# Optimization experiments

Hardware: AMD Instinct MI355X
Metric: run time of the kernel (lower is better)

Reference implementation:

```python
import jax, jax.numpy as jnp
import numpy as np
from jax import lax

D_MODEL = 256
VOCAB = 512
D_INNER = 512          # expand=2
D_STATE = 64
D_CONV = 4
HEADDIM = 32
NHEADS = D_INNER // HEADDIM  # 16
NGROUPS = 1
CHUNK = 64
D_IN_PROJ = 2 * D_INNER + 2 * NGROUPS * D_STATE + NHEADS  # 1168
CONV_DIM = D_INNER + 2 * NGROUPS * D_STATE               # 640


def setup_inputs() -> dict:
    key = jax.random.key(0)
    ks = jax.random.split(key, 8)
    B, L = 8, 4096
    input_ids = jax.random.randint(ks[0], (B, L), 0, VOCAB)
    rn = lambda k, shp, sc: (jax.random.normal(k, shp) * sc).astype(jnp.float32)
    embed_w = rn(ks[1], (VOCAB, D_MODEL), 0.02).at[0].set(0.0)  # padding_idx=0
    in_proj_w = rn(ks[2], (D_IN_PROJ, D_MODEL), D_MODEL ** -0.5)
    conv_w = rn(ks[3], (CONV_DIM, D_CONV), 0.2)
    conv_b = jnp.zeros((CONV_DIM,), jnp.float32)
    A_log = jnp.log(jax.random.uniform(ks[4], (NHEADS,), minval=1.0, maxval=16.0)).astype(jnp.float32)
    D_skip = jnp.ones((NHEADS,), jnp.float32)
    dt0 = jax.random.uniform(ks[5], (NHEADS,), minval=1e-3, maxval=0.1)
    dt_bias = jnp.log(jnp.expm1(dt0)).astype(jnp.float32)  # inverse softplus
    gate_norm_w = jnp.ones((D_INNER,), jnp.float32)
    out_proj_w = rn(ks[6], (D_MODEL, D_INNER), D_INNER ** -0.5)
    norm_w = jnp.ones((D_MODEL,), jnp.float32)
    return dict(input_ids=input_ids, embed_w=embed_w, in_proj_w=in_proj_w,
                conv_w=conv_w, conv_b=conv_b, A_log=A_log, D_skip=D_skip,
                dt_bias=dt_bias, gate_norm_w=gate_norm_w, out_proj_w=out_proj_w,
                norm_w=norm_w)


def _rmsnorm(x, w, eps):
    return x * lax.rsqrt(jnp.mean(x * x, axis=-1, keepdims=True) + eps) * w


def _segsum(a):
    # a: (..., T) -> (..., T, T); out[q,s] = sum_{s+1..q} a, -inf above diag
    T = a.shape[-1]
    c = jnp.cumsum(a, axis=-1)
    seg = c[..., :, None] - c[..., None, :]
    mask = jnp.tril(jnp.ones((T, T), bool))
    return jnp.where(mask, seg, -jnp.inf)


def _ssd(X, A, Bm, Cm):
    # X:(b,l,h,p) already *dt ; A:(b,l,h)=dt*A_head ; Bm,Cm:(b,l,n)
    b, l, h, p = X.shape
    n = Bm.shape[-1]
    c, q = l // CHUNK, CHUNK
    X = X.reshape(b, c, q, h, p)
    A = A.reshape(b, c, q, h).transpose(0, 3, 1, 2)        # (b,h,c,q)
    Bm = Bm.reshape(b, c, q, n)
    Cm = Cm.reshape(b, c, q, n)
    A_cs = jnp.cumsum(A, axis=-1)                           # (b,h,c,q)
    Lmat = jnp.exp(_segsum(A))                              # (b,h,c,q,q)
    # intra-chunk (diagonal block) output
    Y_diag = jnp.einsum('bcqn,bckn,bhcqk,bckhp->bcqhp', Cm, Bm, Lmat, X)
    # states carried to end of each chunk
    decay_states = jnp.exp(A_cs[..., -1:] - A_cs)           # (b,h,c,q)
    states = jnp.einsum('bckn,bhck,bckhp->bchpn', Bm, decay_states, X)
    chunk_decay = jnp.exp(A_cs[..., -1])                    # (b,h,c)
    def step(hprev, inp):
        dec, st = inp
        return dec[..., None, None] * hprev + st, hprev
    _, prev = lax.scan(step, jnp.zeros((b, h, p, n), X.dtype),
                       (chunk_decay.transpose(2, 0, 1), states.transpose(1, 0, 2, 3, 4)))
    prev = prev.transpose(1, 0, 2, 3, 4)                    # (b,c,h,p,n)
    Y_off = jnp.einsum('bcqn,bchpn,bhcq->bcqhp', Cm, prev, jnp.exp(A_cs))
    return (Y_diag + Y_off).reshape(b, l, h, p)


def _mamba2(u, in_proj_w, conv_w, conv_b, A_log, D_skip, dt_bias, gate_norm_w, out_proj_w):
    B, L, _ = u.shape
    zxbcdt = u @ in_proj_w.T                                # (B,L,1168)
    z = zxbcdt[..., :D_INNER]
    xBC = zxbcdt[..., D_INNER:D_INNER + CONV_DIM]
    dt = zxbcdt[..., D_INNER + CONV_DIM:]                   # (B,L,H)
    # causal depthwise conv + silu
    xBC = lax.conv_general_dilated(xBC.transpose(0, 2, 1), conv_w[:, None, :],
                                   (1,), [(D_CONV - 1, 0)],
                                   dimension_numbers=('NCH', 'OIH', 'NCH'),
                                   feature_group_count=CONV_DIM)
    xBC = jax.nn.silu(xBC + conv_b[None, :, None]).transpose(0, 2, 1)
    x = xBC[..., :D_INNER].reshape(B, L, NHEADS, HEADDIM)
    Bm = xBC[..., D_INNER:D_INNER + D_STATE]
    Cm = xBC[..., D_INNER + D_STATE:]
    dt = jax.nn.softplus(dt + dt_bias)                      # (B,L,H)
    A = -jnp.exp(A_log)                                     # (H,)
    y = _ssd(x * dt[..., None], dt * A, Bm, Cm)
    y = y + D_skip[None, None, :, None] * x
    y = y.reshape(B, L, D_INNER)
    y = _rmsnorm(y * jax.nn.silu(z), gate_norm_w, 1e-5)     # RMSNormGated
    return y @ out_proj_w.T


def reference(input_ids, embed_w, in_proj_w, conv_w, conv_b, A_log, D_skip,
              dt_bias, gate_norm_w, out_proj_w, norm_w):
    x = embed_w[input_ids]                                  # (B,L,D)
    u = _rmsnorm(x, norm_w, 1e-6)
    x = x + _mamba2(u, in_proj_w, conv_w, conv_b, A_log, D_skip,
                    dt_bias, gate_norm_w, out_proj_w)
    logits = x @ embed_w.T                                  # tied lm_head
    return logits
```

## Files before the change

### kernel.cpp

```cpp
#include <hip/hip_runtime.h>
#include <cstdint>
#include <cstddef>

#define TOK    32768
#define BATCH  8
#define SEQ    4096
#define DMODEL 256
#define DINNER 512
#define DSTATE 64
#define NH     16
#define HD     32
#define DPROJ  1168
#define NPAD   1280
#define CONVD  640
#define VOCAB  512
#define HGRP   4
#define TS     132

typedef __attribute__((ext_vector_type(8))) short bf16x8;
typedef __attribute__((ext_vector_type(4))) float f32x4;

__device__ __forceinline__ unsigned short f2bf(float f) {
    unsigned u = __float_as_uint(f);
    u += 0x7fffu + ((u >> 16) & 1u);
    return (unsigned short)(u >> 16);
}
__device__ __forceinline__ float bf2f(short s) {
    return __uint_as_float(((unsigned)(unsigned short)s) << 16);
}
__device__ __forceinline__ unsigned cvtpk(float lo, float hi) {
    unsigned r;
    asm("v_cvt_pk_bf16_f32 %0, %1, %2" : "=v"(r) : "v"(lo), "v"(hi));
    return r;
}
__device__ __forceinline__ float fsilu(float s) {
    return s * __builtin_amdgcn_rcpf(1.f + __expf(-s));
}
__device__ __forceinline__ float sp(float v) {
    return v > 20.f ? v : __logf(1.f + __expf(v));
}

__device__ __forceinline__ void gload16(const short* src, short* dst) {
    __builtin_amdgcn_global_load_lds((const __attribute__((address_space(1))) void*)src,
                                     (__attribute__((address_space(3))) void*)dst, 16, 0, 0);
}

#define U16_OFF   0
#define Z16_OFF   (U16_OFF  + (size_t)TOK*128)
#define XBC_OFF   (Z16_OFF  + (size_t)TOK*256)
#define DTS_OFF   (XBC_OFF  + (size_t)TOK*320)
#define ACS_OFF   (DTS_OFF  + (size_t)TOK*16)
#define CDEC_OFF  (ACS_OFF  + (size_t)BATCH*NH*64*64)
#define WP_OFF    (CDEC_OFF + (size_t)BATCH*NH*64)
#define WO_OFF    (WP_OFF   + 163840)
#define WE_OFF    (WO_OFF   + 65536)
#define UNION_OFF (WE_OFF   + 65536)
#define UNION_FL  ((size_t)BATCH*64*NH*2048)
#define Y16_SUB   ((size_t)TOK*256)
#define XF_SUB    ((size_t)TOK*256)
#define WS_FLOATS (UNION_OFF + UNION_FL)

__global__ void k_diag(float* out, float wsmb) {
    if (blockIdx.x == 0 && threadIdx.x == 0) out[0] = wsmb;
}

__global__ void k_cvt(const float* __restrict__ s, short* __restrict__ d, int nsrc, int ntot) {
    int i = blockIdx.x * 256 + threadIdx.x;
    if (i < ntot) d[i] = (i < nsrc) ? (short)f2bf(s[i]) : (short)0;
}

__global__ void k_embed(const int* __restrict__ ids, const float* __restrict__ embed,
                        const float* __restrict__ norm_w, short* __restrict__ u16) {
    int t = blockIdx.x;
    int lane = threadIdx.x;
    int id = ids[t];
    float4 v = ((const float4*)(embed + (size_t)id * DMODEL))[lane];
    float ss = v.x*v.x + v.y*v.y + v.z*v.z + v.w*v.w;
    #pragma unroll
    for (int o = 32; o > 0; o >>= 1) ss += __shfl_down(ss, o);
    ss = __shfl(ss, 0);
    float r = rsqrtf(ss * (1.0f / DMODEL) + 1e-6f);
    float4 w = ((const float4*)norm_w)[lane];
    unsigned p0 = cvtpk(v.x * r * w.x, v.y * r * w.y);
    unsigned p1 = cvtpk(v.z * r * w.z, v.w * r * w.w);
    ((uint2*)(u16 + (size_t)t * DMODEL))[lane] = make_uint2(p0, p1);
}

template<int MODE>
__global__ __launch_bounds__(512) void k_gemm_mfma(
    const short* __restrict__ A, const short* __restrict__ B, int K,
    float* __restrict__ outF, short* __restrict__ z16, short* __restrict__ xbc,
    float* __restrict__ dts, const float* __restrict__ dt_bias,
    const int* __restrict__ ids, const float* __restrict__ embed,
    const float* __restrict__ cw, const float* __restrict__ cb) {
    __shared__ __align__(16) short SM[32768];
    int tid = threadIdx.x;
    int m0 = blockIdx.y << 7;
    int n0 = blockIdx.x << 7;
    int wave = tid >> 6, lane = tid & 63;
    int wm = wave >> 1, wn = wave & 1;
    int lr = lane & 15, lg = lane >> 4;
    const f32x4 zer = {0.f, 0.f, 0.f, 0.f};
    f32x4 acc[2][4];
    #pragma unroll
    for (int i = 0; i < 2; i++)
        #pragma unroll
        for (int j = 0; j < 4; j++) acc[i][j] = zer;

    const bool isXBC = (MODE == 0) && (n0 >= 512) && (n0 < 1152);
    const bool atStart = (m0 & (SEQ - 1)) == 0;
    const bool haloLane = isXBC && (wm == 0) && !atStart && (lr < 3);
    f32x4 hacc[4];
    #pragma unroll
    for (int j = 0; j < 4; j++) hacc[j] = zer;
    const bf16x8 hz = {0, 0, 0, 0, 0, 0, 0, 0};
    bf16x8 hc0 = hz, hc1 = hz, hn0 = hz, hn1 = hz;

    const int nK = K >> 6;
    const int slo = lane >> 3;
    const int skb = ((lane & 7) ^ slo) << 3;

    {
        #pragma unroll
        for (int j = 0; j < 2; j++) {
            int row = wave * 16 + j * 8 + slo;
            gload16(A + (size_t)(m0 + row) * K + skb, SM + (wave * 2 + j) * 512);
            gload16(B + (size_t)(n0 + row) * K + skb, SM + 16384 + (wave * 2 + j) * 512);
        }
        if (haloLane) {
            hc0 = *(const bf16x8*)(A + (size_t)(m0 - 3 + lr) * K + lg * 8);
            hc1 = *(const bf16x8*)(A + (size_t)(m0 - 3 + lr) * K + 32 + lg * 8);
        }
    }
    __syncthreads();

    for (int kt = 0; kt < nK; ++kt) {
        if (kt + 1 < nK) {
            int k0 = (kt + 1) << 6;
            int nb = ((kt + 1) & 1) * 8192;
            #pragma unroll
            for (int j = 0; j < 2; j++) {
                int row = wave * 16 + j * 8 + slo;
                gload16(A + (size_t)(m0 + row) * K + k0 + skb, SM + nb + (wave * 2 + j) * 512);
                gload16(B + (size_t)(n0 + row) * K + k0 + skb, SM + 16384 + nb + (wave * 2 + j) * 512);
            }
            if (haloLane) {
                hn0 = *(const bf16x8*)(A + (size_t)(m0 - 3 + lr) * K + k0 + lg * 8);
                hn1 = *(const bf16x8*)(A + (size_t)(m0 - 3 + lr) * K + k0 + 32 + lg * 8);
            }
        }
        const short* CA = SM + (kt & 1) * 8192;
        const short* CB = SM + 16384 + (kt & 1) * 8192;
        #pragma unroll
        for (int kk = 0; kk < 2; kk++) {
            int sw = (((kk << 2) + lg) ^ (lr & 7)) << 3;
            bf16x8 af[2], bfr[4];
            #pragma unroll
            for (int mi = 0; mi < 2; mi++)
                af[mi] = *(const bf16x8*)&CA[(wm * 32 + mi * 16 + lr) * 64 + sw];
            #pragma unroll
            for (int ni = 0; ni < 4; ni++)
                bfr[ni] = *(const bf16x8*)&CB[(wn * 64 + ni * 16 + lr) * 64 + sw];
            #pragma unroll
            for (int mi = 0; mi < 2; mi++)
                #pragma unroll
                for (int ni = 0; ni < 4; ni++)
                    acc[mi][ni] = __builtin_amdgcn_mfma_f32_16x16x32_bf16(af[mi], bfr[ni], acc[mi][ni], 0, 0, 0);
            if (isXBC && wm == 0) {
                bf16x8 h = (kk == 0) ? hc0 : hc1;
                #pragma unroll
                for (int ni = 0; ni < 4; ni++)
                    hacc[ni] = __builtin_amdgcn_mfma_f32_16x16x32_bf16(h, bfr[ni], hacc[ni], 0, 0, 0);
            }
        }
        __syncthreads();
        hc0 = hn0; hc1 = hn1;
    }

    if (isXBC) {
        short* Tile = SM;
        #pragma unroll
        for (int mi = 0; mi < 2; mi++)
            #pragma unroll
            for (int ni = 0; ni < 4; ni++)
                #pragma unroll
                for (int r = 0; r < 4; r++) {
                    int row = wm * 32 + mi * 16 + lg * 4 + r;
                    int col = wn * 64 + ni * 16 + lr;
                    float v = acc[mi][ni][r];
                    float vo = __shfl_xor(v, 1);
                    if (!(lr & 1))
                        *(unsigned*)&Tile[(3 + row) * TS + col] = cvtpk(v, vo);
                }
        if (wm == 0 && lg == 0) {
            #pragma unroll
            for (int ni = 0; ni < 4; ni++)
                #pragma unroll
                for (int r = 0; r < 3; r++)
                    Tile[r * TS + wn * 64 + ni * 16 + lr] = (short)f2bf(hacc[ni][r]);
        }
        __syncthreads();
        int cp = tid & 63, rg = tid >> 6;
        int colb = cp * 2;
        int ch = (n0 - 512) + colb;
        float c0w0 = cw[ch * 4], c0w1 = cw[ch * 4 + 1], c0w2 = cw[ch * 4 + 2], c0w3 = cw[ch * 4 + 3];
        float c1w0 = cw[ch * 4 + 4], c1w1 = cw[ch * 4 + 5], c1w2 = cw[ch * 4 + 6], c1w3 = cw[ch * 4 + 7];
        float b0v = cb[ch], b1v = cb[ch + 1];
        int rbase = rg * 16;
        unsigned w0 = *(const unsigned*)&Tile[(rbase + 0) * TS + colb];
        unsigned w1 = *(const unsigned*)&Tile[(rbase + 1) * TS + colb];
        unsigned w2 = *(const unsigned*)&Tile[(rbase + 2) * TS + colb];
        for (int i = 0; i < 16; i++) {
            unsigned w3 = *(const unsigned*)&Tile[(rbase + i + 3) * TS + colb];
            float s0 = b0v, s1 = b1v;
            s0 = fmaf(bf2f((short)(w0 & 0xffffu)), c0w0, s0); s1 = fmaf(bf2f((short)(w0 >> 16)), c1w0, s1);
            s0 = fmaf(bf2f((short)(w1 & 0xffffu)), c0w1, s0); s1 = fmaf(bf2f((short)(w1 >> 16)), c1w1, s1);
            s0 = fmaf(bf2f((short)(w2 & 0xffffu)), c0w2, s0); s1 = fmaf(bf2f((short)(w2 >> 16)), c1w2, s1);
            s0 = fmaf(bf2f((short)(w3 & 0xffffu)), c0w3, s0); s1 = fmaf(bf2f((short)(w3 >> 16)), c1w3, s1);
            s0 = fsilu(s0);
            s1 = fsilu(s1);
            *(unsigned*)&xbc[(size_t)(m0 + rbase + i) * CONVD + ch] = cvtpk(s0, s1);
            w0 = w1; w1 = w2; w2 = w3;
        }
        return;
    }

    #pragma unroll
    for (int mi = 0; mi < 2; mi++) {
        #pragma unroll
        for (int r = 0; r < 4; r++) {
            int row = m0 + wm * 32 + mi * 16 + lg * 4 + r;
            int id = 0;
            if (MODE == 1) id = ids[row];
            #pragma unroll
            for (int ni = 0; ni < 4; ni++) {
                int col = n0 + wn * 64 + ni * 16 + lr;
                float v = acc[mi][ni][r];
                if (MODE == 0) {
                    if (n0 < 512) {
                        float vo = __shfl_xor(v, 1);
                        if (!(lr & 1))
                            *(unsigned*)&z16[(size_t)row * DINNER + col] = cvtpk(v, vo);
                    } else if (wn == 0 && ni == 0) {
                        dts[(size_t)row * NH + lr] = sp(v + dt_bias[lr]);
                    }
                } else if (MODE == 1) {
                    float vo = __shfl_xor(v, 1);
                    if (!(lr & 1)) {
                        float2 res = *(const float2*)&embed[(size_t)id * DMODEL + col];
                        *(unsigned*)&z16[(size_t)row * DMODEL + col] = cvtpk(v + res.x, vo + res.y);
                    }
                } else {
                    outF[(size_t)row * VOCAB + col] = v;
                }
            }
        }
    }
}

__global__ __launch_bounds__(256) void k_states(const short* __restrict__ xbc, const float* __restrict__ dts,
                                                const float* __restrict__ A_log,
                                                short* __restrict__ st16,
                                                float* __restrict__ acs_g, float* __restrict__ cdec) {
    __shared__ short BsB[64 * 72];
    __shared__ short BT[64 * 72];
    __shared__ short Xd0[32 * 72];
    __shared__ short Xd1[32 * 72];
    __shared__ float dkS[HGRP][64];
    int tid = threadIdx.x;
    int bid = blockIdx.x;
    int hg = bid & 3;
    int bc = bid >> 2;
    int b = bc >> 6, c = bc & 63;
    int h0 = hg * HGRP;
    size_t tbase = (size_t)b * SEQ + (size_t)c * 64;
    int wave = tid >> 6, lane = tid & 63;
    int lr = lane & 15, lg = lane >> 4;

    for (int i = tid; i < 64 * 64; i += 256) {
        int q = i >> 6, n = i & 63;
        BsB[q * 72 + n] = xbc[(tbase + q) * CONVD + DINNER + n];
    }
    {
        int h = h0 + wave;
        float Ah = -__expf(A_log[h]);
        float v = dts[(tbase + lane) * NH + h] * Ah;
        #pragma unroll
        for (int off = 1; off < 64; off <<= 1) {
            float o = __shfl_up(v, off);
            if (lane >= off) v += o;
        }
        acs_g[(((size_t)(b * NH + h)) * 64 + c) * 64 + lane] = v;
        float alast = __shfl(v, 63);
        dkS[wave][lane] = __expf(alast - v);
        if (lane == 0) cdec[(b * NH + h) * 64 + c] = __expf(alast);
    }
    __syncthreads();
    for (int i = tid; i < 64 * 64; i += 256) {
        int k = i >> 6, n = i & 63;
        BT[n * 72 + k] = BsB[k * 72 + n];
    }
    __syncthreads();

    auto do_head = [&](int h, const short* Xd) {
        int ptile = wave & 1;
        bf16x8 a0 = *(const bf16x8*)&Xd[(ptile * 16 + lr) * 72 + lg * 8];
        bf16x8 a1 = *(const bf16x8*)&Xd[(ptile * 16 + lr) * 72 + 32 + lg * 8];
        size_t base = ((size_t)bc * NH + h) * 2048;
        #pragma unroll
        for (int j = 0; j < 2; j++) {
            int nt = (wave >> 1) * 2 + j;
            bf16x8 b0 = *(const bf16x8*)&BT[(nt * 16 + lr) * 72 + lg * 8];
            bf16x8 b1 = *(const bf16x8*)&BT[(nt * 16 + lr) * 72 + 32 + lg * 8];
            f32x4 z = {0.f, 0.f, 0.f, 0.f};
            z = __builtin_amdgcn_mfma_f32_16x16x32_bf16(a0, b0, z, 0, 0, 0);
            z = __builtin_amdgcn_mfma_f32_16x16x32_bf16(a1, b1, z, 0, 0, 0);
            #pragma unroll
            for (int r = 0; r < 4; r++) {
                int p = ptile * 16 + lg * 4 + r;
                float v = z[r];
                float vo = __shfl_xor(v, 1);
                if (!(lr & 1))
                    *(unsigned*)&st16[base + p * 64 + nt * 16 + lr] = cvtpk(v, vo);
            }
        }
    };

    #pragma unroll
    for (int pr = 0; pr < HGRP / 2; pr++) {
        int hhA = pr * 2, hhB = hhA + 1;
        int hA = h0 + hhA, hB = h0 + hhB;
        for (int i = tid; i < 2048; i += 256) {
            int p = i & 31, k = i >> 5;
            float dtA = dts[(tbase + k) * NH + hA];
            float dtB = dts[(tbase + k) * NH + hB];
            Xd0[p * 72 + k] = (short)f2bf(bf2f(xbc[(tbase + k) * CONVD + hA * HD + p]) * dtA * dkS[hhA][k]);
            Xd1[p * 72 + k] = (short)f2bf(bf2f(xbc[(tbase + k) * CONVD + hB * HD + p]) * dtB * dkS[hhB][k]);
        }
        __syncthreads();
        do_head(hA, Xd0);
        do_head(hB, Xd1);
        __syncthreads();
    }
}

__global__ __launch_bounds__(256) void k_scan(unsigned* __restrict__ st32, const float* __restrict__ cdec) {
    int bid = blockIdx.x;
    int bh = bid >> 2, seg = bid & 3;
    int b = bh >> 4, h = bh & 15;
    int off = seg * 256 + threadIdx.x;
    float p0 = 0.f, p1 = 0.f;
    for (int c = 0; c < 64; c++) {
        float dec = cdec[bh * 64 + c];
        size_t idx = ((((size_t)b * 64 + c) * NH) + h) * 1024 + off;
        unsigned v = st32[idx];
        float s0 = bf2f((short)(v & 0xffffu));
        float s1 = bf2f((short)(v >> 16));
        st32[idx] = cvtpk(p0, p1);
        p0 = fmaf(dec, p0, s0);
        p1 = fmaf(dec, p1, s1);
    }
}

__global__ __launch_bounds__(256) void k_y(const short* __restrict__ xbc, const float* __restrict__ dts,
                                           const short* __restrict__ st16, const float* __restrict__ acs_g,
                                           const float* __restrict__ D_skip, short* __restrict__ Y16) {
    __shared__ short CsB[64 * 72];
    __shared__ short Wsh[64 * 72];
    __shared__ short XtS[32 * 72];
    __shared__ short Pt[32 * 72];
    __shared__ float acsS[HGRP][64];
    int tid = threadIdx.x;
    int bid = blockIdx.x;
    int hg = bid & 3;
    int bc = bid >> 2;
    int b = bc >> 6, c = bc & 63;
    int h0 = hg * HGRP;
    size_t tbase = (size_t)b * SEQ + (size_t)c * 64;
    int wave = tid >> 6, lane = tid & 63;
    int lr = lane & 15, lg = lane >> 4;

    for (int i = tid; i < 64 * 64; i += 256) {
        int q = i >> 6, n = i & 63;
        const short* rowp = xbc + (tbase + q) * CONVD + DINNER;
        Wsh[q * 72 + n] = rowp[n];
        CsB[q * 72 + n] = rowp[DSTATE + n];
    }
    acsS[wave][lane] = acs_g[(((size_t)(b * NH + h0 + wave)) * 64 + c) * 64 + lane];
    __syncthreads();

    f32x4 macc[4];
    bf16x8 ca0 = *(const bf16x8*)&CsB[(wave * 16 + lr) * 72 + lg * 8];
    bf16x8 ca1 = *(const bf16x8*)&CsB[(wave * 16 + lr) * 72 + 32 + lg * 8];
    {
        #pragma unroll
        for (int ct = 0; ct < 4; ct++) {
            bf16x8 b0 = *(const bf16x8*)&Wsh[(ct * 16 + lr) * 72 + lg * 8];
            bf16x8 b1 = *(const bf16x8*)&Wsh[(ct * 16 + lr) * 72 + 32 + lg * 8];
            f32x4 z = {0.f, 0.f, 0.f, 0.f};
            z = __builtin_amdgcn_mfma_f32_16x16x32_bf16(ca0, b0, z, 0, 0, 0);
            z = __builtin_amdgcn_mfma_f32_16x16x32_bf16(ca1, b1, z, 0, 0, 0);
            macc[ct] = z;
        }
    }
    __syncthreads();

    for (int hh = 0; hh < HGRP; hh++) {
        int h = h0 + hh;
        #pragma unroll
        for (int ct = 0; ct < 4; ct++) {
            int k = ct * 16 + lr;
            #pragma unroll
            for (int r = 0; r < 4; r++) {
                int q = wave * 16 + lg * 4 + r;
                float wv = 0.f;
                if (k <= q) wv = macc[ct][r] * __expf(acsS[hh][q] - acsS[hh][k]);
                float wo = __shfl_xor(wv, 1);
                if (!(lr & 1))
                    *(unsigned*)&Wsh[q * 72 + k] = cvtpk(wv, wo);
            }
        }
        for (int i = tid; i < 2048; i += 256) {
            int p = i & 31, k = i >> 5;
            float xv = bf2f(xbc[(tbase + k) * CONVD + h * HD + p]);
            XtS[p * 72 + k] = (short)f2bf(xv * dts[(tbase + k) * NH + h]);
        }
        size_t sbase = ((size_t)bc * NH + h) * 2048;
        for (int i = tid; i < 2048; i += 256)
            Pt[(i >> 6) * 72 + (i & 63)] = st16[sbase + i];
        __syncthreads();
        float eq[4];
        #pragma unroll
        for (int r = 0; r < 4; r++) eq[r] = __expf(acsS[hh][wave * 16 + lg * 4 + r]);
        float dsk = D_skip[h];
        bf16x8 wa0 = *(const bf16x8*)&Wsh[(wave * 16 + lr) * 72 + lg * 8];
        bf16x8 wa1 = *(const bf16x8*)&Wsh[(wave * 16 + lr) * 72 + 32 + lg * 8];
        #pragma unroll
        for (int pt = 0; pt < 2; pt++) {
            bf16x8 xb0 = *(const bf16x8*)&XtS[(pt * 16 + lr) * 72 + lg * 8];
            bf16x8 xb1 = *(const bf16x8*)&XtS[(pt * 16 + lr) * 72 + 32 + lg * 8];
            f32x4 zd = {0.f, 0.f, 0.f, 0.f};
            zd = __builtin_amdgcn_mfma_f32_16x16x32_bf16(wa0, xb0, zd, 0, 0, 0);
            zd = __builtin_amdgcn_mfma_f32_16x16x32_bf16(wa1, xb1, zd, 0, 0, 0);
            bf16x8 pb0 = *(const bf16x8*)&Pt[(pt * 16 + lr) * 72 + lg * 8];
            bf16x8 pb1 = *(const bf16x8*)&Pt[(pt * 16 + lr) * 72 + 32 + lg * 8];
            f32x4 zo = {0.f, 0.f, 0.f, 0.f};
            zo = __builtin_amdgcn_mfma_f32_16x16x32_bf16(ca0, pb0, zo, 0, 0, 0);
            zo = __builtin_amdgcn_mfma_f32_16x16x32_bf16(ca1, pb1, zo, 0, 0, 0);
            #pragma unroll
            for (int r = 0; r < 4; r++) {
                int q = wave * 16 + lg * 4 + r;
                int p = pt * 16 + lr;
                float xv = bf2f(xbc[(tbase + q) * CONVD + h * HD + p]);
                float v = zd[r] + eq[r] * zo[r] + dsk * xv;
                float vo = __shfl_xor(v, 1);
                if (!(lr & 1))
                    *(unsigned*)&Y16[((tbase + q) * NH + h) * HD + p] = cvtpk(v, vo);
            }
        }
        __syncthreads();
    }
}

__global__ void k_gate(const short* __restrict__ Y16, const short* __restrict__ z16,
                       const float* __restrict__ gw, short* __restrict__ Yb) {
    int t = blockIdx.x;
    int lane = threadIdx.x;
    union { int4 v; short s[8]; } zu, yu;
    zu.v = *(const int4*)(z16 + (size_t)t * DINNER + lane * 8);
    yu.v = *(const int4*)(Y16 + (size_t)t * DINNER + lane * 8);
    float g[8];
    float ss = 0.f;
    #pragma unroll
    for (int i = 0; i < 8; i++) {
        float zf = bf2f(zu.s[i]);
        g[i] = bf2f(yu.s[i]) * fsilu(zf);
        ss += g[i] * g[i];
    }
    #pragma unroll
    for (int o = 32; o > 0; o >>= 1) ss += __shfl_down(ss, o);
    ss = __shfl(ss, 0);
    float rr = rsqrtf(ss * (1.0f / DINNER) + 1e-5f);
    const float* wr = gw + lane * 8;
    float4 w0 = *(const float4*)wr;
    float4 w1 = *(const float4*)(wr + 4);
    float wv[8] = {w0.x, w0.y, w0.z, w0.w, w1.x, w1.y, w1.z, w1.w};
    union { uint4 v; unsigned u[4]; } ou;
    #pragma unroll
    for (int i = 0; i < 4; i++)
        ou.u[i] = cvtpk(g[2*i] * rr * wv[2*i], g[2*i+1] * rr * wv[2*i+1]);
    *(uint4*)(Yb + (size_t)t * DINNER + lane * 8) = ou.v;
}

extern "C" void kernel_launch(void* const* d_in, const int* in_sizes, int n_in,
                              void* d_out, int out_size, void* d_ws, size_t ws_size,
                              hipStream_t stream) {
    const int*   ids        = (const int*)d_in[0];
    const float* embed_w    = (const float*)d_in[1];
    const float* in_proj_w  = (const float*)d_in[2];
    const float* conv_w     = (const float*)d_in[3];
    const float* conv_b     = (const float*)d_in[4];
    const float* A_log      = (const float*)d_in[5];
    const float* D_skip     = (const float*)d_in[6];
    const float* dt_bias    = (const float*)d_in[7];
    const float* gate_w     = (const float*)d_in[8];
    const float* out_proj_w = (const float*)d_in[9];
    const float* norm_w     = (const float*)d_in[10];
    float* out = (float*)d_out;

    if (ws_size < WS_FLOATS * sizeof(float)) {
        k_diag<<<1, 64, 0, stream>>>(out, (float)(ws_size >> 20));
        return;
    }

    float* ws   = (float*)d_ws;
    short* u16  = (short*)(ws + U16_OFF);
    short* z16  = (short*)(ws + Z16_OFF);
    short* xbc  = (short*)(ws + XBC_OFF);
    float* dts  = ws + DTS_OFF;
    float* acs  = ws + ACS_OFF;
    float* cdec = ws + CDEC_OFF;
    short* Wp   = (short*)(ws + WP_OFF);
    short* Wo   = (short*)(ws + WO_OFF);
    short* We   = (short*)(ws + WE_OFF);
    short* st16 = (short*)(ws + UNION_OFF);
    short* Y16  = (short*)(ws + UNION_OFF + Y16_SUB);
    short* Yb   = (short*)(ws + UNION_OFF);
    short* xf16 = (short*)(ws + UNION_OFF + XF_SUB);

    k_cvt<<<(NPAD * DMODEL + 255) / 256, 256, 0, stream>>>(in_proj_w, Wp, DPROJ * DMODEL, NPAD * DMODEL);
    k_cvt<<<(DMODEL * DINNER + 255) / 256, 256, 0, stream>>>(out_proj_w, Wo, DMODEL * DINNER, DMODEL * DINNER);
    k_cvt<<<(VOCAB * DMODEL + 255) / 256, 256, 0, stream>>>(embed_w, We, VOCAB * DMODEL, VOCAB * DMODEL);
    k_embed<<<TOK, 64, 0, stream>>>(ids, embed_w, norm_w, u16);
    k_gemm_mfma<0><<<dim3(NPAD / 128, TOK / 128), 512, 0, stream>>>(
        u16, Wp, DMODEL, nullptr, z16, xbc, dts, dt_bias, nullptr, nullptr, conv_w, conv_b);
    k_states<<<BATCH * 64 * 4, 256, 0, stream>>>(xbc, dts, A_log, st16, acs, cdec);
    k_scan<<<BATCH * NH * 4, 256, 0, stream>>>((unsigned*)st16, cdec);
    k_y<<<BATCH * 64 * 4, 256, 0, stream>>>(xbc, dts, st16, acs, D_skip, Y16);
    k_gate<<<TOK, 64, 0, stream>>>(Y16, z16, gate_w, Yb);
    k_gemm_mfma<1><<<dim3(DMODEL / 128, TOK / 128), 512, 0, stream>>>(
        Yb, Wo, DINNER, nullptr, xf16, nullptr, nullptr, nullptr, ids, embed_w, nullptr, nullptr);
    k_gemm_mfma<2><<<dim3(VOCAB / 128, TOK / 128), 512, 0, stream>>>(
        xf16, We, DMODEL, out, nullptr, nullptr, nullptr, nullptr, nullptr, nullptr, nullptr, nullptr);
}
```

Baseline: 246.6 us.

## Stage x and chunk states via 16-byte LDS loads with XOR-swizzled state layout

In k_states and k_y, each head's x slice (64 tokens x 32 dims) is now fetched with 16-byte gload16 copies into LDS, and per-head dt and A-cumsum values are staged in shared arrays. Strided scalar global gathers are replaced by LDS reads. Chunk states are written in an XOR-swizzled layout so k_y can copy them straight into a padless LDS buffer and read bf16x8 fragments without bank conflicts. k_states now handles one head per iteration instead of two, which adds barriers per block in exchange for lower global-load cost.

```diff
diff --git a/kernel.cpp b/kernel.cpp
--- a/kernel.cpp
+++ b/kernel.cpp
@@ -264,9 +264,10 @@
                                                 float* __restrict__ acs_g, float* __restrict__ cdec) {
     __shared__ short BsB[64 * 72];
     __shared__ short BT[64 * 72];
-    __shared__ short Xd0[32 * 72];
-    __shared__ short Xd1[32 * 72];
+    __shared__ short XdS[32 * 72];
+    __shared__ __align__(16) short XKP[64 * 32];
     __shared__ float dkS[HGRP][64];
+    __shared__ float dtS[64];
     int tid = threadIdx.x;
     int bid = blockIdx.x;
     int hg = bid & 3;
@@ -300,46 +301,45 @@
         int k = i >> 6, n = i & 63;
         BT[n * 72 + k] = BsB[k * 72 + n];
     }
-    __syncthreads();
-
-    auto do_head = [&](int h, const short* Xd) {
-        int ptile = wave & 1;
-        bf16x8 a0 = *(const bf16x8*)&Xd[(ptile * 16 + lr) * 72 + lg * 8];
-        bf16x8 a1 = *(const bf16x8*)&Xd[(ptile * 16 + lr) * 72 + 32 + lg * 8];
-        size_t base = ((size_t)bc * NH + h) * 2048;
-        #pragma unroll
-        for (int j = 0; j < 2; j++) {
-            int nt = (wave >> 1) * 2 + j;
-            bf16x8 b0 = *(const bf16x8*)&BT[(nt * 16 + lr) * 72 + lg * 8];
-            bf16x8 b1 = *(const bf16x8*)&BT[(nt * 16 + lr) * 72 + 32 + lg * 8];
-            f32x4 z = {0.f, 0.f, 0.f, 0.f};
-            z = __builtin_amdgcn_mfma_f32_16x16x32_bf16(a0, b0, z, 0, 0, 0);
-            z = __builtin_amdgcn_mfma_f32_16x16x32_bf16(a1, b1, z, 0, 0, 0);
-            #pragma unroll
-            for (int r = 0; r < 4; r++) {
-                int p = ptile * 16 + lg * 4 + r;
-                float v = z[r];
-                float vo = __shfl_xor(v, 1);
-                if (!(lr & 1))
-                    *(unsigned*)&st16[base + p * 64 + nt * 16 + lr] = cvtpk(v, vo);
-            }
-        }
-    };
-
-    #pragma unroll
-    for (int pr = 0; pr < HGRP / 2; pr++) {
-        int hhA = pr * 2, hhB = hhA + 1;
-        int hA = h0 + hhA, hB = h0 + hhB;
+
+    for (int hh = 0; hh < HGRP; hh++) {
+        int h = h0 + hh;
+        {
+            int s = wave * 64 + lane;
+            gload16(xbc + (tbase + (s >> 2)) * CONVD + h * HD + (s & 3) * 8, XKP + wave * 512);
+        }
+        if (tid < 64) dtS[tid] = dts[(tbase + tid) * NH + h];
+        __syncthreads();
         for (int i = tid; i < 2048; i += 256) {
             int p = i & 31, k = i >> 5;
-            float dtA = dts[(tbase + k) * NH + hA];
-            float dtB = dts[(tbase + k) * NH + hB];
-            Xd0[p * 72 + k] = (short)f2bf(bf2f(xbc[(tbase + k) * CONVD + hA * HD + p]) * dtA * dkS[hhA][k]);
-            Xd1[p * 72 + k] = (short)f2bf(bf2f(xbc[(tbase + k) * CONVD + hB * HD + p]) * dtB * dkS[hhB][k]);
-        }
-        __syncthreads();
-        do_head(hA, Xd0);
-        do_head(hB, Xd1);
+            XdS[p * 72 + k] = (short)f2bf(bf2f(XKP[k * 32 + p]) * dtS[k] * dkS[hh][k]);
+        }
+        __syncthreads();
+        {
+            int ptile = wave & 1;
+            bf16x8 a0 = *(const bf16x8*)&XdS[(ptile * 16 + lr) * 72 + lg * 8];
+            bf16x8 a1 = *(const bf16x8*)&XdS[(ptile * 16 + lr) * 72 + 32 + lg * 8];
+            size_t base = ((size_t)bc * NH + h) * 2048;
+            #pragma unroll
+            for (int j = 0; j < 2; j++) {
+                int nt = (wave >> 1) * 2 + j;
+                bf16x8 b0 = *(const bf16x8*)&BT[(nt * 16 + lr) * 72 + lg * 8];
+                bf16x8 b1 = *(const bf16x8*)&BT[(nt * 16 + lr) * 72 + 32 + lg * 8];
+                f32x4 z = {0.f, 0.f, 0.f, 0.f};
+                z = __builtin_amdgcn_mfma_f32_16x16x32_bf16(a0, b0, z, 0, 0, 0);
+                z = __builtin_amdgcn_mfma_f32_16x16x32_bf16(a1, b1, z, 0, 0, 0);
+                #pragma unroll
+                for (int r = 0; r < 4; r++) {
+                    int p = ptile * 16 + lg * 4 + r;
+                    float v = z[r];
+                    float vo = __shfl_xor(v, 1);
+                    if (!(lr & 1)) {
+                        int chunk = (nt << 1) | (lr >> 3);
+                        *(unsigned*)&st16[base + p * 64 + ((chunk ^ (p & 7)) << 3) + (lr & 7)] = cvtpk(v, vo);
+                    }
+                }
+            }
+        }
         __syncthreads();
     }
 }
@@ -368,8 +368,10 @@
     __shared__ short CsB[64 * 72];
     __shared__ short Wsh[64 * 72];
     __shared__ short XtS[32 * 72];
-    __shared__ short Pt[32 * 72];
-    __shared__ float acsS[HGRP][64];
+    __shared__ __align__(16) short PtL[32 * 64];
+    __shared__ __align__(16) short XKP[64 * 32];
+    __shared__ float acsH[64];
+    __shared__ float dtS[64];
     int tid = threadIdx.x;
     int bid = blockIdx.x;
     int hg = bid & 3;
@@ -386,7 +388,6 @@
         Wsh[q * 72 + n] = rowp[n];
         CsB[q * 72 + n] = rowp[DSTATE + n];
     }
-    acsS[wave][lane] = acs_g[(((size_t)(b * NH + h0 + wave)) * 64 + c) * 64 + lane];
     __syncthreads();
 
     f32x4 macc[4];
@@ -407,6 +408,16 @@
 
     for (int hh = 0; hh < HGRP; hh++) {
         int h = h0 + hh;
+        {
+            int s = wave * 64 + lane;
+            gload16(xbc + (tbase + (s >> 2)) * CONVD + h * HD + (s & 3) * 8, XKP + wave * 512);
+            gload16(st16 + ((size_t)bc * NH + h) * 2048 + s * 8, PtL + wave * 512);
+        }
+        if (tid < 64) {
+            acsH[tid] = acs_g[(((size_t)(b * NH + h)) * 64 + c) * 64 + tid];
+            dtS[tid] = dts[(tbase + tid) * NH + h];
+        }
+        __syncthreads();
         #pragma unroll
         for (int ct = 0; ct < 4; ct++) {
             int k = ct * 16 + lr;
@@ -414,7 +425,7 @@
             for (int r = 0; r < 4; r++) {
                 int q = wave * 16 + lg * 4 + r;
                 float wv = 0.f;
-                if (k <= q) wv = macc[ct][r] * __expf(acsS[hh][q] - acsS[hh][k]);
+                if (k <= q) wv = macc[ct][r] * __expf(acsH[q] - acsH[k]);
                 float wo = __shfl_xor(wv, 1);
                 if (!(lr & 1))
                     *(unsigned*)&Wsh[q * 72 + k] = cvtpk(wv, wo);
@@ -422,36 +433,32 @@
         }
         for (int i = tid; i < 2048; i += 256) {
             int p = i & 31, k = i >> 5;
-            float xv = bf2f(xbc[(tbase + k) * CONVD + h * HD + p]);
-            XtS[p * 72 + k] = (short)f2bf(xv * dts[(tbase + k) * NH + h]);
-        }
-        size_t sbase = ((size_t)bc * NH + h) * 2048;
-        for (int i = tid; i < 2048; i += 256)
-            Pt[(i >> 6) * 72 + (i & 63)] = st16[sbase + i];
+            XtS[p * 72 + k] = (short)f2bf(bf2f(XKP[k * 32 + p]) * dtS[k]);
+        }
         __syncthreads();
         float eq[4];
         #pragma unroll
-        for (int r = 0; r < 4; r++) eq[r] = __expf(acsS[hh][wave * 16 + lg * 4 + r]);
+        for (int r = 0; r < 4; r++) eq[r] = __expf(acsH[wave * 16 + lg * 4 + r]);
         float dsk = D_skip[h];
         bf16x8 wa0 = *(const bf16x8*)&Wsh[(wave * 16 + lr) * 72 + lg * 8];
         bf16x8 wa1 = *(const bf16x8*)&Wsh[(wave * 16 + lr) * 72 + 32 + lg * 8];
         #pragma unroll
         for (int pt = 0; pt < 2; pt++) {
-            bf16x8 xb0 = *(const bf16x8*)&XtS[(pt * 16 + lr) * 72 + lg * 8];
-            bf16x8 xb1 = *(const bf16x8*)&XtS[(pt * 16 + lr) * 72 + 32 + lg * 8];
+            int p = pt * 16 + lr;
+            bf16x8 xb0 = *(const bf16x8*)&XtS[p * 72 + lg * 8];
+            bf16x8 xb1 = *(const bf16x8*)&XtS[p * 72 + 32 + lg * 8];
             f32x4 zd = {0.f, 0.f, 0.f, 0.f};
             zd = __builtin_amdgcn_mfma_f32_16x16x32_bf16(wa0, xb0, zd, 0, 0, 0);
             zd = __builtin_amdgcn_mfma_f32_16x16x32_bf16(wa1, xb1, zd, 0, 0, 0);
-            bf16x8 pb0 = *(const bf16x8*)&Pt[(pt * 16 + lr) * 72 + lg * 8];
-            bf16x8 pb1 = *(const bf16x8*)&Pt[(pt * 16 + lr) * 72 + 32 + lg * 8];
+            bf16x8 pb0 = *(const bf16x8*)&PtL[p * 64 + ((lg ^ (p & 7)) << 3)];
+            bf16x8 pb1 = *(const bf16x8*)&PtL[p * 64 + (((lg + 4) ^ (p & 7)) << 3)];
             f32x4 zo = {0.f, 0.f, 0.f, 0.f};
             zo = __builtin_amdgcn_mfma_f32_16x16x32_bf16(ca0, pb0, zo, 0, 0, 0);
             zo = __builtin_amdgcn_mfma_f32_16x16x32_bf16(ca1, pb1, zo, 0, 0, 0);
             #pragma unroll
             for (int r = 0; r < 4; r++) {
                 int q = wave * 16 + lg * 4 + r;
-                int p = pt * 16 + lr;
-                float xv = bf2f(xbc[(tbase + q) * CONVD + h * HD + p]);
+                float xv = bf2f(XKP[q * 32 + p]);
                 float v = zd[r] + eq[r] * zo[r] + dsk * xv;
                 float vo = __shfl_xor(v, 1);
                 if (!(lr & 1))
```

After: 222.1 us. 1.11x faster.
